# Kernel optimization log

Hardware: AMD Instinct MI355X
Metric: run time of the kernel (lower is better)

## Reference

```python
import jax, jax.numpy as jnp
import numpy as np

D_MODEL = 1024
N_HEADS = 16
D_HEAD = D_MODEL // N_HEADS
B, T = 4, 2048


def setup_inputs() -> dict:
    key = jax.random.key(0)
    ks = jax.random.split(key, 5)
    s = 1.0 / np.sqrt(D_MODEL)
    x = jax.random.normal(ks[0], (B, T, D_MODEL), dtype=jnp.float32)
    Wq = jax.random.uniform(ks[1], (D_MODEL, D_MODEL), jnp.float32, -s, s)
    Wk = jax.random.uniform(ks[2], (D_MODEL, D_MODEL), jnp.float32, -s, s)
    Wv = jax.random.uniform(ks[3], (D_MODEL, D_MODEL), jnp.float32, -s, s)
    Wo = jax.random.uniform(ks[4], (D_MODEL, D_MODEL), jnp.float32, -s, s)
    # causal mask, 0 = masked (matches torch masked_fill(mask == 0, -inf))
    mask = jnp.tril(jnp.ones((T, T), dtype=jnp.int32))[None, None, :, :]
    return {"x": x, "Wq": Wq, "Wk": Wk, "Wv": Wv, "Wo": Wo, "mask": mask}


def reference(x, Wq, Wk, Wv, Wo, mask):
    def split_heads(t):  # [B,T,D] -> [B,H,T,d]
        return t.reshape(B, T, N_HEADS, D_HEAD).transpose(0, 2, 1, 3)

    Q = split_heads(x @ Wq.T)
    K = split_heads(x @ Wk.T)
    V = split_heads(x @ Wv.T)
    scale = 1.0 / np.sqrt(D_HEAD).astype(np.float32)
    attn = jnp.einsum('bhqd,bhkd->bhqk', Q, K) * scale
    attn = jnp.where(mask == 0, -jnp.inf, attn)
    attn = jax.nn.softmax(attn, axis=-1)
    out = jnp.einsum('bhqk,bhkd->bhqd', attn, V)
    out = out.transpose(0, 2, 1, 3).reshape(B, T, D_MODEL)
    return out @ Wo.T
```

## Files before the change

### kernel.cpp

```cpp
#include <hip/hip_runtime.h>
#include <hip/hip_bf16.h>
#include <cstdint>

#define T_SEQ   2048
#define DMODEL  1024
#define NHEADS  16
#define DHEAD   64
#define B_SZ    4
#define M_ROWS  (B_SZ * T_SEQ)
#define QSCALE  0.1803368801111204f

typedef unsigned short u16;
typedef __attribute__((ext_vector_type(8))) __bf16 bf16x8;
typedef __attribute__((ext_vector_type(4))) float  f32x4;

__device__ __forceinline__ u16 f2bf(float f) {
  uint32_t u = __float_as_uint(f);
  u += 0x7FFF + ((u >> 16) & 1);
  return (u16)(u >> 16);
}

__device__ __forceinline__ float fast_exp2(float x) {
  return __builtin_amdgcn_exp2f(x);
}

__device__ __forceinline__ void gload_lds16(const void* g, void* l) {
  __builtin_amdgcn_global_load_lds(
      (const __attribute__((address_space(1))) void*)g,
      (__attribute__((address_space(3))) void*)l, 16, 0, 0);
}

#define BAR  __builtin_amdgcn_s_barrier()
#define LG0  asm volatile("s_waitcnt lgkmcnt(0)" ::: "memory")
#define VM4  asm volatile("s_waitcnt vmcnt(4)" ::: "memory")
#define VM0  asm volatile("s_waitcnt vmcnt(0)" ::: "memory")
#define PRIO1 __builtin_amdgcn_s_setprio(1)
#define PRIO0 __builtin_amdgcn_s_setprio(0)

__global__ void cvt_all(const float* __restrict__ x,  const float* __restrict__ Wq,
                        const float* __restrict__ Wk, const float* __restrict__ Wv,
                        const float* __restrict__ Wo, u16* __restrict__ xb,
                        u16* __restrict__ Wb) {
  const int NX = (B_SZ * T_SEQ * DMODEL) / 8;
  const int NW = (DMODEL * DMODEL) / 8;
  int i = blockIdx.x * blockDim.x + threadIdx.x;
  int stride = gridDim.x * blockDim.x;
  for (; i < NX + 4 * NW; i += stride) {
    const float* src; u16* dst; int idx;
    if (i < NX) { src = x; dst = xb; idx = i; }
    else {
      int j = i - NX, w = j >> 17;
      idx = j & (NW - 1);
      src = (w == 0) ? Wq : (w == 1) ? Wk : (w == 2) ? Wv : Wo;
      dst = Wb + (size_t)w * (DMODEL * DMODEL);
    }
    const float4* s4 = (const float4*)src;
    float4 a = s4[2 * idx], b = s4[2 * idx + 1];
    union { u16 u[8]; uint4 v; } o;
    o.u[0] = f2bf(a.x); o.u[1] = f2bf(a.y); o.u[2] = f2bf(a.z); o.u[3] = f2bf(a.w);
    o.u[4] = f2bf(b.x); o.u[5] = f2bf(b.y); o.u[6] = f2bf(b.z); o.u[7] = f2bf(b.w);
    ((uint4*)dst)[idx] = o.v;
  }
}

__global__ __launch_bounds__(512, 2) void gemm8p_qkv(
    const u16* __restrict__ A, const u16* __restrict__ Wall,
    u16* __restrict__ Qb, u16* __restrict__ Kb, u16* __restrict__ Vtb) {
  constexpr int K = DMODEL;
  __shared__ u16 As[2][2][128 * 64];
  __shared__ u16 Bs[2][2][128 * 64];
  const int tid = threadIdx.x;
  const int wid = tid >> 6, lane = tid & 63;
  const int wr = wid >> 2, wc = wid & 3;
  const int flat = blockIdx.x;
  const int xcd = flat & 7, serial = flat >> 3;
  const int tm = (serial / 12) * 8 + xcd;
  const int tn = serial % 12;
  const int lrow = lane & 15, lq = lane >> 4;
  const int sr = lrow & 7;
  const int srow = tid >> 3;
  const int csw = ((tid & 7) ^ (srow & 7)) * 8;
  const int cha = (tid & 7) * 8;

  const u16* Arow = A    + (size_t)(tm * 256 + srow) * K + csw;
  const u16* Wrow = Wall + (size_t)(tn * 256 + srow) * K + csw;

  auto stageA = [&](int kt, int d, int h) {
    gload_lds16(Arow + (size_t)(h * 128) * K + kt,      &As[d][h][srow * 64 + cha]);
    gload_lds16(Arow + (size_t)(h * 128 + 64) * K + kt, &As[d][h][(64 + srow) * 64 + cha]);
  };
  auto stageB = [&](int kt, int d, int h) {
    gload_lds16(Wrow + (size_t)(h * 128) * K + kt,      &Bs[d][h][srow * 64 + cha]);
    gload_lds16(Wrow + (size_t)(h * 128 + 64) * K + kt, &Bs[d][h][(64 + srow) * 64 + cha]);
  };

  f32x4 acc[8][4];
#pragma unroll
  for (int m = 0; m < 8; m++)
#pragma unroll
    for (int n = 0; n < 4; n++) acc[m][n] = f32x4{0.f, 0.f, 0.f, 0.f};

  auto ldA = [&](bf16x8 (&a)[4][2], int d, int mb) {
#pragma unroll
    for (int m = 0; m < 4; m++)
#pragma unroll
      for (int kk = 0; kk < 2; kk++)
        a[m][kk] = *(const bf16x8*)&As[d][wr][((mb + m) * 16 + lrow) * 64 + (((kk * 4 + lq) ^ sr) * 8)];
  };
  auto ldB = [&](bf16x8 (&b)[2][2], int d, int nb) {
#pragma unroll
    for (int n = 0; n < 2; n++)
#pragma unroll
      for (int kk = 0; kk < 2; kk++)
        b[n][kk] = *(const bf16x8*)&Bs[d][wc >> 1][((wc & 1) * 64 + (nb + n) * 16 + lrow) * 64 + (((kk * 4 + lq) ^ sr) * 8)];
  };
  auto quad = [&](bf16x8 (&a)[4][2], bf16x8 (&b)[2][2], int mb, int nb) {
#pragma unroll
    for (int m = 0; m < 4; m++)
#pragma unroll
      for (int n = 0; n < 2; n++)
#pragma unroll
        for (int kk = 0; kk < 2; kk++)
          acc[mb + m][nb + n] =
              __builtin_amdgcn_mfma_f32_16x16x32_bf16(a[m][kk], b[n][kk], acc[mb + m][nb + n], 0, 0, 0);
  };

  stageB(0, 0, 0); stageB(0, 0, 1);
  stageA(0, 0, 0); stageA(0, 0, 1);
  stageB(64, 1, 0); stageB(64, 1, 1);
  VM4;
  BAR;

#pragma unroll
  for (int i = 0; i < 8; ++i) {
    const int t1 = 2 * i + 1, u0 = 2 * i + 2, u1 = 2 * i + 3;
    bf16x8 aq0[4][2], aq1[4][2], bq0[2][2], bq1[2][2];
    ldA(aq0, 0, 0); ldB(bq0, 0, 0);
    stageA(t1 * 64, 1, 0);
    BAR; LG0; PRIO1; quad(aq0, bq0, 0, 0); PRIO0; BAR;
    ldB(bq1, 0, 2);
    stageA(t1 * 64, 1, 1);
    BAR; LG0; PRIO1; quad(aq0, bq1, 0, 2); PRIO0; BAR;
    ldA(aq1, 0, 4);
    if (u0 < 16) stageB(u0 * 64, 0, 0);
    BAR; LG0; PRIO1; quad(aq1, bq1, 4, 2); PRIO0; BAR;
    if (u0 < 16) stageB(u0 * 64, 0, 1);
    BAR; PRIO1; quad(aq1, bq0, 4, 0); PRIO0;
    if (i < 7) { VM4; } else { VM0; }
    BAR;
    ldA(aq0, 1, 0); ldB(bq0, 1, 0);
    if (u0 < 16) stageA(u0 * 64, 0, 0);
    BAR; LG0; PRIO1; quad(aq0, bq0, 0, 0); PRIO0; BAR;
    ldB(bq1, 1, 2);
    if (u0 < 16) stageA(u0 * 64, 0, 1);
    BAR; LG0; PRIO1; quad(aq0, bq1, 0, 2); PRIO0; BAR;
    ldA(aq1, 1, 4);
    if (u1 < 16) stageB(u1 * 64, 1, 0);
    BAR; LG0; PRIO1; quad(aq1, bq1, 4, 2); PRIO0; BAR;
    if (u1 < 16) stageB(u1 * 64, 1, 1);
    BAR; PRIO1; quad(aq1, bq0, 4, 0); PRIO0;
    if (i < 7) { VM4; }
    BAR;
  }

  const int y = tn >> 2;
  const int hcol = (tn & 3) * 4 + wc;
  u16* dst = (y == 0) ? Qb : (y == 1) ? Kb : Vtb;
  const float scale = (y == 0) ? QSCALE : 1.0f;
#pragma unroll
  for (int m = 0; m < 8; m++)
#pragma unroll
    for (int n = 0; n < 4; n++)
#pragma unroll
      for (int v = 0; v < 4; v++) {
        int i_ = tm * 256 + wr * 128 + m * 16 + lq * 4 + v;
        int d_ = n * 16 + lrow;
        int b_ = i_ >> 11, t_ = i_ & 2047;
        float val = acc[m][n][v] * scale;
        if (y == 2)
          dst[((size_t)(b_ * NHEADS + hcol) * 64 + d_) * T_SEQ + t_] = f2bf(val);
        else
          dst[((size_t)(b_ * NHEADS + hcol) * T_SEQ + t_) * 64 + d_] = f2bf(val);
      }
}

__global__ __launch_bounds__(256) void gemm3(
    const u16* __restrict__ A, const u16* __restrict__ Wall,
    float* __restrict__ C0) {
  constexpr int K = DMODEL;
  constexpr int NTILES = K / 64;
  constexpr int NT = 8;
  __shared__ u16 As[2][128 * 64];
  __shared__ u16 Bs[2][128 * 64];
  const int tid = threadIdx.x;
  const int wid = tid >> 6, lane = tid & 63;
  const int flat = blockIdx.x;
  const int xcd = flat & 7, serial = flat >> 3;
  const int tm = (serial / NT) * 8 + xcd;
  const int tn = serial % NT;
  const int wr = wid >> 1, wc = wid & 1;
  const int lrow = lane & 15, lq = lane >> 4;
  const int sr = lrow & 7;
  const int srow = lane >> 3;
  const int csw = ((lane & 7) ^ srow) * 8;

  const u16* Arow = A    + (size_t)(tm * 128 + srow) * K + csw;
  const u16* Wrow = Wall + (size_t)(tn * 128 + srow) * K + csw;

  auto stage = [&](int k0, int b) {
#pragma unroll
    for (int it = 0; it < 4; ++it) {
      int rbase = it * 32 + wid * 8;
      gload_lds16(Arow + (size_t)rbase * K + k0, &As[b][rbase * 64]);
      gload_lds16(Wrow + (size_t)rbase * K + k0, &Bs[b][rbase * 64]);
    }
  };

  f32x4 acc[4][4];
#pragma unroll
  for (int m = 0; m < 4; m++)
#pragma unroll
    for (int n = 0; n < 4; n++) acc[m][n] = f32x4{0.f, 0.f, 0.f, 0.f};

  auto compute = [&](int b) {
#pragma unroll
    for (int kk = 0; kk < 2; ++kk) {
      bf16x8 a[4], bb[4];
      const int co = ((kk * 4 + lq) ^ sr) * 8;
#pragma unroll
      for (int m = 0; m < 4; m++)
        a[m] = *(const bf16x8*)&As[b][(wr * 64 + m * 16 + lrow) * 64 + co];
#pragma unroll
      for (int n = 0; n < 4; n++)
        bb[n] = *(const bf16x8*)&Bs[b][(wc * 64 + n * 16 + lrow) * 64 + co];
#pragma unroll
      for (int m = 0; m < 4; m++)
#pragma unroll
        for (int n = 0; n < 4; n++)
          acc[m][n] = __builtin_amdgcn_mfma_f32_16x16x32_bf16(a[m], bb[n], acc[m][n], 0, 0, 0);
    }
  };

  stage(0, 0);
  stage(64, 1);
  asm volatile("s_waitcnt vmcnt(8)" ::: "memory");
  __builtin_amdgcn_s_barrier();

  for (int t = 0; t < NTILES; t += 2) {
    compute(0);
    asm volatile("" ::: "memory");
    __builtin_amdgcn_s_barrier();
    if (t + 2 < NTILES) {
      stage((t + 2) * 64, 0);
      asm volatile("s_waitcnt vmcnt(8)" ::: "memory");
    } else {
      asm volatile("s_waitcnt vmcnt(0)" ::: "memory");
    }
    __builtin_amdgcn_s_barrier();
    compute(1);
    if (t + 3 < NTILES) {
      asm volatile("" ::: "memory");
      __builtin_amdgcn_s_barrier();
      stage((t + 3) * 64, 1);
      asm volatile("s_waitcnt vmcnt(8)" ::: "memory");
      __builtin_amdgcn_s_barrier();
    }
  }

#pragma unroll
  for (int m = 0; m < 4; m++)
#pragma unroll
    for (int n = 0; n < 4; n++)
#pragma unroll
      for (int v = 0; v < 4; v++) {
        int i = tm * 128 + wr * 64 + m * 16 + lq * 4 + v;
        int j = tn * 128 + wc * 64 + n * 16 + lrow;
        C0[(size_t)i * DMODEL + j] = acc[m][n][v];
      }
}

__global__ __launch_bounds__(256) void flash_attn(
    const u16* __restrict__ Q, const u16* __restrict__ Kg,
    const u16* __restrict__ Vt, u16* __restrict__ Ao) {
  __shared__ u16 Ks[2][64 * 64];
  __shared__ u16 Vs[2][64 * 64];
  __shared__ u16 Ps[4][16 * 64];
  const int tid = threadIdx.x, wid = tid >> 6, lane = tid & 63;
  const int flat = blockIdx.x;
  const int serial = flat >> 3;
  const int bh = (serial >> 4) * 8 + (flat & 7);
  const int qi = serial & 15;
  const int qtA = qi, qtB = 31 - qi;
  const int lrow = lane & 15, lq = lane >> 4;
  const int sr = lrow & 7;
  const int srow = lane >> 3;
  const int csw = ((lane & 7) ^ srow) * 8;

  const u16* qbase = Q + ((size_t)bh * T_SEQ + wid * 16 + lrow) * 64 + lq * 8;
  const bf16x8 qA0 = *(const bf16x8*)(qbase + (size_t)qtA * 4096);
  const bf16x8 qA1 = *(const bf16x8*)(qbase + (size_t)qtA * 4096 + 32);
  const bf16x8 qB0 = *(const bf16x8*)(qbase + (size_t)qtB * 4096);
  const bf16x8 qB1 = *(const bf16x8*)(qbase + (size_t)qtB * 4096 + 32);

  bf16x8 ones;
  {
    union { u16 u; __bf16 b; } c; c.u = 0x3F80;
#pragma unroll
    for (int j = 0; j < 8; j++) ones[j] = c.b;
  }

  f32x4 poA[4], poB[4], lA, lB;
#pragma unroll
  for (int n = 0; n < 4; n++) { poA[n] = f32x4{0.f,0.f,0.f,0.f}; poB[n] = f32x4{0.f,0.f,0.f,0.f}; }
  lA = f32x4{0.f,0.f,0.f,0.f}; lB = f32x4{0.f,0.f,0.f,0.f};

  auto stage = [&](int kt, int b) {
#pragma unroll
    for (int it = 0; it < 2; ++it) {
      int rbase = it * 32 + wid * 8;
      gload_lds16(Kg + ((size_t)bh * T_SEQ + kt * 64 + rbase + srow) * 64 + csw,
                  &Ks[b][rbase * 64]);
      gload_lds16(Vt + ((size_t)bh * 64 + rbase + srow) * T_SEQ + kt * 64 + csw,
                  &Vs[b][rbase * 64]);
    }
  };

  stage(0, 0);
  __syncthreads();
  int cur = 0;

  for (int kt = 0; kt <= qtB; ++kt) {
    if (kt < qtB) stage(kt + 1, cur ^ 1);

    bf16x8 kf0[4], kf1[4];
#pragma unroll
    for (int n = 0; n < 4; n++) {
      kf0[n] = *(const bf16x8*)&Ks[cur][(n * 16 + lrow) * 64 + ((lq ^ sr) * 8)];
      kf1[n] = *(const bf16x8*)&Ks[cur][(n * 16 + lrow) * 64 + (((lq + 4) ^ sr) * 8)];
    }

    auto apply = [&](const bf16x8& q0, const bf16x8& q1,
                     f32x4 (&po)[4], f32x4& l4, bool diag) {
      f32x4 s[4];
#pragma unroll
      for (int n = 0; n < 4; n++) {
        f32x4 a = f32x4{0.f, 0.f, 0.f, 0.f};
        a = __builtin_amdgcn_mfma_f32_16x16x32_bf16(q0, kf0[n], a, 0, 0, 0);
        a = __builtin_amdgcn_mfma_f32_16x16x32_bf16(q1, kf1[n], a, 0, 0, 0);
        s[n] = a;
      }
      if (diag) {
#pragma unroll
        for (int n = 0; n < 4; n++)
#pragma unroll
          for (int v = 0; v < 4; v++) {
            int kcol = n * 16 + lrow;
            int qrow = wid * 16 + lq * 4 + v;
            if (kcol > qrow) s[n][v] = -1e30f;
          }
      }
#pragma unroll
      for (int n = 0; n < 4; n++)
#pragma unroll
        for (int v = 0; v < 4; v++) {
          float p = fast_exp2(s[n][v]);
          int col = n * 16 + lrow;
          int r = lq * 4 + v;
          Ps[wid][r * 64 + (((col >> 3) ^ (r & 7)) * 8) + (col & 7)] =
              (u16)(__float_as_uint(p) >> 16);
        }
#pragma unroll
      for (int kk = 0; kk < 2; kk++) {
        bf16x8 pa = *(const bf16x8*)&Ps[wid][lrow * 64 + (((kk * 4 + lq) ^ sr) * 8)];
#pragma unroll
        for (int n = 0; n < 4; n++) {
          bf16x8 vf = *(const bf16x8*)&Vs[cur][(n * 16 + lrow) * 64 + (((kk * 4 + lq) ^ sr) * 8)];
          po[n] = __builtin_amdgcn_mfma_f32_16x16x32_bf16(pa, vf, po[n], 0, 0, 0);
        }
        l4 = __builtin_amdgcn_mfma_f32_16x16x32_bf16(pa, ones, l4, 0, 0, 0);
      }
    };

    if (kt <= qtA) apply(qA0, qA1, poA, lA, kt == qtA);
    apply(qB0, qB1, poB, lB, kt == qtB);

    asm volatile("s_waitcnt vmcnt(0)" ::: "memory");
    __syncthreads();
    cur ^= 1;
  }

  const int b_ = bh >> 4, h_ = bh & 15;
  auto epi = [&](int qt_, f32x4 (&po)[4], f32x4& l4) {
    float rl[4];
#pragma unroll
    for (int v = 0; v < 4; v++) rl[v] = 1.0f / l4[v];
#pragma unroll
    for (int n = 0; n < 4; n++)
#pragma unroll
      for (int v = 0; v < 4; v++) {
        int t_ = qt_ * 64 + wid * 16 + lq * 4 + v;
        int col = h_ * 64 + n * 16 + lrow;
        Ao[((size_t)b_ * T_SEQ + t_) * DMODEL + col] = f2bf(po[n][v] * rl[v]);
      }
  };
  epi(qtA, poA, lA);
  epi(qtB, poB, lB);
}

extern "C" void kernel_launch(void* const* d_in, const int* in_sizes, int n_in,
                              void* d_out, int out_size, void* d_ws, size_t ws_size,
                              hipStream_t stream) {
  const float* x  = (const float*)d_in[0];
  const float* Wq = (const float*)d_in[1];
  const float* Wk = (const float*)d_in[2];
  const float* Wv = (const float*)d_in[3];
  const float* Wo = (const float*)d_in[4];
  float* out = (float*)d_out;

  char* ws = (char*)d_ws;
  u16* xb  = (u16*)(ws);
  u16* Wb  = (u16*)(ws + 16777216);
  u16* Qb  = (u16*)(ws + 25165824);
  u16* Kb  = (u16*)(ws + 41943040);
  u16* Vtb = (u16*)(ws + 58720256);
  u16* Aob = xb;

  cvt_all<<<2048, 256, 0, stream>>>(x, Wq, Wk, Wv, Wo, xb, Wb);

  gemm8p_qkv<<<384, 512, 0, stream>>>(xb, Wb, Qb, Kb, Vtb);

  flash_attn<<<1024, 256, 0, stream>>>(Qb, Kb, Vtb, Aob);

  gemm3<<<512, 256, 0, stream>>>(Aob, Wb + 3 * 1048576, out);
}
```

Measured before the change: 193.0 us.

## Process four query tiles per attention block to share K/V tile loads

Each flash-attention block now handles four query tiles (iq, 31-iq, 15-iq, 16+iq) instead of two, reusing every staged K/V tile across all four. The grid is halved from 1024 to 512 blocks while causal work stays balanced per block. This cuts global K/V traffic and LDS staging per unit of work. In exchange it roughly doubles accumulator and Q-fragment register pressure, which may lower occupancy, and leaves fewer blocks to fill the GPU.

Result: faster. 186.0 us (-3.6%).

```diff
diff --git a/kernel.cpp b/kernel.cpp
--- a/kernel.cpp
+++ b/kernel.cpp
@@ -287,20 +287,23 @@
   __shared__ u16 Ps[4][16 * 64];
   const int tid = threadIdx.x, wid = tid >> 6, lane = tid & 63;
   const int flat = blockIdx.x;
-  const int serial = flat >> 3;
-  const int bh = (serial >> 4) * 8 + (flat & 7);
-  const int qi = serial & 15;
-  const int qtA = qi, qtB = 31 - qi;
+  const int xcd = flat & 7, serial = flat >> 3;
+  const int iq = serial & 7;
+  const int bh = (serial >> 3) * 8 + xcd;
+  int qt[4] = { iq, 31 - iq, 15 - iq, 16 + iq };
+  const int kmax = 31 - iq;
   const int lrow = lane & 15, lq = lane >> 4;
   const int sr = lrow & 7;
   const int srow = lane >> 3;
   const int csw = ((lane & 7) ^ srow) * 8;
 
   const u16* qbase = Q + ((size_t)bh * T_SEQ + wid * 16 + lrow) * 64 + lq * 8;
-  const bf16x8 qA0 = *(const bf16x8*)(qbase + (size_t)qtA * 4096);
-  const bf16x8 qA1 = *(const bf16x8*)(qbase + (size_t)qtA * 4096 + 32);
-  const bf16x8 qB0 = *(const bf16x8*)(qbase + (size_t)qtB * 4096);
-  const bf16x8 qB1 = *(const bf16x8*)(qbase + (size_t)qtB * 4096 + 32);
+  bf16x8 qf0[4], qf1[4];
+#pragma unroll
+  for (int j = 0; j < 4; j++) {
+    qf0[j] = *(const bf16x8*)(qbase + (size_t)qt[j] * 4096);
+    qf1[j] = *(const bf16x8*)(qbase + (size_t)qt[j] * 4096 + 32);
+  }
 
   bf16x8 ones;
   {
@@ -309,10 +312,13 @@
     for (int j = 0; j < 8; j++) ones[j] = c.b;
   }
 
-  f32x4 poA[4], poB[4], lA, lB;
-#pragma unroll
-  for (int n = 0; n < 4; n++) { poA[n] = f32x4{0.f,0.f,0.f,0.f}; poB[n] = f32x4{0.f,0.f,0.f,0.f}; }
-  lA = f32x4{0.f,0.f,0.f,0.f}; lB = f32x4{0.f,0.f,0.f,0.f};
+  f32x4 po[4][4], l4[4];
+#pragma unroll
+  for (int j = 0; j < 4; j++) {
+#pragma unroll
+    for (int n = 0; n < 4; n++) po[j][n] = f32x4{0.f, 0.f, 0.f, 0.f};
+    l4[j] = f32x4{0.f, 0.f, 0.f, 0.f};
+  }
 
   auto stage = [&](int kt, int b) {
 #pragma unroll
@@ -329,8 +335,8 @@
   __syncthreads();
   int cur = 0;
 
-  for (int kt = 0; kt <= qtB; ++kt) {
-    if (kt < qtB) stage(kt + 1, cur ^ 1);
+  for (int kt = 0; kt <= kmax; ++kt) {
+    if (kt < kmax) stage(kt + 1, cur ^ 1);
 
     bf16x8 kf0[4], kf1[4];
 #pragma unroll
@@ -340,7 +346,7 @@
     }
 
     auto apply = [&](const bf16x8& q0, const bf16x8& q1,
-                     f32x4 (&po)[4], f32x4& l4, bool diag) {
+                     f32x4 (&poj)[4], f32x4& lj, bool diag) {
       f32x4 s[4];
 #pragma unroll
       for (int n = 0; n < 4; n++) {
@@ -375,14 +381,15 @@
 #pragma unroll
         for (int n = 0; n < 4; n++) {
           bf16x8 vf = *(const bf16x8*)&Vs[cur][(n * 16 + lrow) * 64 + (((kk * 4 + lq) ^ sr) * 8)];
-          po[n] = __builtin_amdgcn_mfma_f32_16x16x32_bf16(pa, vf, po[n], 0, 0, 0);
+          poj[n] = __builtin_amdgcn_mfma_f32_16x16x32_bf16(pa, vf, poj[n], 0, 0, 0);
         }
-        l4 = __builtin_amdgcn_mfma_f32_16x16x32_bf16(pa, ones, l4, 0, 0, 0);
+        lj = __builtin_amdgcn_mfma_f32_16x16x32_bf16(pa, ones, lj, 0, 0, 0);
       }
     };
 
-    if (kt <= qtA) apply(qA0, qA1, poA, lA, kt == qtA);
-    apply(qB0, qB1, poB, lB, kt == qtB);
+#pragma unroll
+    for (int j = 0; j < 4; j++)
+      if (kt <= qt[j]) apply(qf0[j], qf1[j], po[j], l4[j], kt == qt[j]);
 
     asm volatile("s_waitcnt vmcnt(0)" ::: "memory");
     __syncthreads();
@@ -390,21 +397,20 @@
   }
 
   const int b_ = bh >> 4, h_ = bh & 15;
-  auto epi = [&](int qt_, f32x4 (&po)[4], f32x4& l4) {
+#pragma unroll
+  for (int j = 0; j < 4; j++) {
     float rl[4];
 #pragma unroll
-    for (int v = 0; v < 4; v++) rl[v] = 1.0f / l4[v];
+    for (int v = 0; v < 4; v++) rl[v] = 1.0f / l4[j][v];
 #pragma unroll
     for (int n = 0; n < 4; n++)
 #pragma unroll
       for (int v = 0; v < 4; v++) {
-        int t_ = qt_ * 64 + wid * 16 + lq * 4 + v;
+        int t_ = qt[j] * 64 + wid * 16 + lq * 4 + v;
         int col = h_ * 64 + n * 16 + lrow;
-        Ao[((size_t)b_ * T_SEQ + t_) * DMODEL + col] = f2bf(po[n][v] * rl[v]);
-      }
-  };
-  epi(qtA, poA, lA);
-  epi(qtB, poB, lB);
+        Ao[((size_t)b_ * T_SEQ + t_) * DMODEL + col] = f2bf(po[j][n][v] * rl[v]);
+      }
+  }
 }
 
 extern "C" void kernel_launch(void* const* d_in, const int* in_sizes, int n_in,
@@ -429,7 +435,7 @@
 
   gemm8p_qkv<<<384, 512, 0, stream>>>(xb, Wb, Qb, Kb, Vtb);
 
-  flash_attn<<<1024, 256, 0, stream>>>(Qb, Kb, Vtb, Aob);
+  flash_attn<<<512, 256, 0, stream>>>(Qb, Kb, Vtb, Aob);
 
   gemm3<<<512, 256, 0, stream>>>(Aob, Wb + 3 * 1048576, out);
 }
```
